# Kernel optimization log

Hardware: AMD Instinct MI355X
Metric: run time of the kernel (lower is better)

The kernel has to match this reference:

```python
import jax, jax.numpy as jnp
import numpy as np

# Module constants (from init_kwargs)
X_RANGE = (-10.0, 10.0)
Y_RANGE = (-10.0, 10.0)
N_X = 64
N_Y = 64
B = 16
N_CTX = 1024


def make_grid():
    # x counted forward, y counted backwards (image-row convention):
    # grid[k*N_X + j] = (xs[j], ys[k]) with ys from max to min.
    xs = jnp.linspace(X_RANGE[0], X_RANGE[1], N_X, dtype=jnp.float32)
    ys = jnp.linspace(Y_RANGE[1], Y_RANGE[0], N_Y, dtype=jnp.float32)
    gx, gy = jnp.meshgrid(xs, ys)          # each (N_Y, N_X)
    return jnp.stack([gx, gy], axis=-1).reshape(-1, 2)  # (G, 2)


def setup_inputs() -> dict:
    key = jax.random.key(0)
    k1, k2 = jax.random.split(key)
    X = jax.random.uniform(k1, (B, N_CTX, 2), dtype=jnp.float32,
                           minval=X_RANGE[0], maxval=X_RANGE[1])
    Y = jax.random.normal(k2, (B, N_CTX, 2), dtype=jnp.float32)
    log_l_scale = jnp.zeros((), dtype=jnp.float32)  # log(1.0)
    return {"X": X, "Y": Y, "log_l_scale": log_l_scale}


def reference(X, Y, log_l_scale):
    grid = make_grid()                                  # (G, 2)
    l = jnp.exp(log_l_scale)
    # squared distances via expansion to avoid a (B,G,n,2) intermediate
    g2 = jnp.sum(grid * grid, axis=-1)                  # (G,)
    x2 = jnp.sum(X * X, axis=-1)                        # (B, n)
    gx = jnp.einsum('gd,bnd->bgn', grid, X)             # (B, G, n)
    d2 = g2[None, :, None] + x2[:, None, :] - 2.0 * gx  # (B, G, n)
    Gram = jnp.exp(-0.5 * d2 / (l * l))                 # RBF kernel, B=1
    # expand Y with a leading ones (density) channel
    ones = jnp.ones(Y.shape[:2] + (1,), dtype=Y.dtype)
    EY = jnp.concatenate([ones, Y], axis=-1)            # (B, n, 3)
    FM = jnp.einsum('bgn,bnc->bgc', Gram, EY)           # (B, G, 3)
    dens = FM[..., 0:1]
    FM = jnp.concatenate([dens, FM[..., 1:] / dens], axis=-1)
    # (B, G, 3) -> (B, 3, N_Y, N_X)
    return FM.reshape(X.shape[0], N_Y, N_X, 3).transpose(0, 3, 1, 2)
```

## Files before the change

### kernel.cpp

```cpp
#include <hip/hip_runtime.h>
#include <hip/hip_bf16.h>
#include <math.h>

#define NB    16
#define NCTX  1024
#define NXG   64
#define NG    4096
#define GT_PER_B 16

__global__ __launch_bounds__(256)
void equiv_encoder_kernel(const float* __restrict__ X,
                          const float* __restrict__ Y,
                          const float* __restrict__ log_l_scale,
                          float* __restrict__ out) {
    const int b  = blockIdx.x >> 4;
    const int gt = blockIdx.x & 15;
    const int g  = gt * 256 + threadIdx.x;
    const int ix = g & 63;
    const int iy = g >> 6;

    const float step = 20.0f / 63.0f;
    const float gx = -10.0f + step * (float)ix;
    const float gy =  10.0f - step * (float)iy;

    const float logl  = log_l_scale[0];
    const float scale = -0.72134752044448170f * expf(-2.0f * logl);

    __shared__ float4 s[NCTX];
    const float2* Xb = (const float2*)(X + (size_t)b * NCTX * 2);
    const float2* Yb = (const float2*)(Y + (size_t)b * NCTX * 2);
    for (int i = threadIdx.x; i < NCTX; i += 256) {
        float2 xv = Xb[i];
        float2 yv = Yb[i];
        s[i] = make_float4(xv.x, xv.y, yv.x, yv.y);
    }
    __syncthreads();

    float a0 = 0.0f, a1 = 0.0f, a2 = 0.0f;
#pragma unroll 8
    for (int n = 0; n < NCTX; ++n) {
        float4 v = s[n];
        float dx = gx - v.x;
        float dy = gy - v.y;
        float d2 = fmaf(dx, dx, dy * dy);
        float w  = exp2f(d2 * scale);
        a0 += w;
        a1 = fmaf(w, v.z, a1);
        a2 = fmaf(w, v.w, a2);
    }

    const float inv = 1.0f / a0;
    float* ob = out + (size_t)b * 3 * NG;
    ob[g]            = a0;
    ob[NG + g]       = a1 * inv;
    ob[2 * NG + g]   = a2 * inv;
}

extern "C" void kernel_launch(void* const* d_in, const int* in_sizes, int n_in,
                              void* d_out, int out_size, void* d_ws, size_t ws_size,
                              hipStream_t stream) {
    const float* X    = (const float*)d_in[0];
    const float* Y    = (const float*)d_in[1];
    const float* logl = (const float*)d_in[2];
    float* out = (float*)d_out;

    dim3 grid(NB * GT_PER_B);
    dim3 block(256);
    equiv_encoder_kernel<<<grid, block, 0, stream>>>(X, Y, logl, out);
}
```

Measured before the change: 89.95 us.

## Factor RBF into separable x/y exponentials and split context across blocks

Uses the separability of the Gaussian on a regular grid, exp(-(dx²+dy²)) = exp(-dx²)·exp(-dy²), so per-axis weights are precomputed into shared memory and the inner loop becomes pure FMAs with no per-pair exp. Each thread now computes a 2x2 grid patch. The context dimension is split into 16 chunks across 1024 blocks, and a second kernel reduces the partials from workspace and normalizes. This removes the exp-bound inner loop and raises parallelism, in exchange for a second launch and workspace traffic.

```diff
diff --git a/kernel.cpp b/kernel.cpp
--- a/kernel.cpp
+++ b/kernel.cpp
@@ -2,58 +2,98 @@
 #include <hip/hip_bf16.h>
 #include <math.h>
 
-#define NB    16
-#define NCTX  1024
-#define NXG   64
-#define NG    4096
-#define GT_PER_B 16
+
+#define NB     16
+#define NCTX   1024
+#define NG     4096
+#define NC     64
+#define NSPLIT 16
+#define GQ     4
 
 __global__ __launch_bounds__(256)
-void equiv_encoder_kernel(const float* __restrict__ X,
-                          const float* __restrict__ Y,
-                          const float* __restrict__ log_l_scale,
-                          float* __restrict__ out) {
-    const int b  = blockIdx.x >> 4;
-    const int gt = blockIdx.x & 15;
-    const int g  = gt * 256 + threadIdx.x;
-    const int ix = g & 63;
-    const int iy = g >> 6;
+void ee_partial(const float* __restrict__ X,
+                const float* __restrict__ Y,
+                const float* __restrict__ log_l_scale,
+                float* __restrict__ ws) {
+    const int blk = blockIdx.x;
+    const int b   = blk >> 6;
+    const int r   = blk & 63;
+    const int gq  = r >> 4;
+    const int nc  = r & 15;
+    const int n0  = nc * NC;
+    const int iy0 = gq * 16;
 
-    const float step = 20.0f / 63.0f;
-    const float gx = -10.0f + step * (float)ix;
-    const float gy =  10.0f - step * (float)iy;
+    const float step  = 20.0f / 63.0f;
+    const float scale = -0.72134752044448170f * expf(-2.0f * log_l_scale[0]);
 
-    const float logl  = log_l_scale[0];
-    const float scale = -0.72134752044448170f * expf(-2.0f * logl);
+    __shared__ float  wx[NC][64];
+    __shared__ float  wy[NC][16];
+    __shared__ float2 sy[NC];
 
-    __shared__ float4 s[NCTX];
     const float2* Xb = (const float2*)(X + (size_t)b * NCTX * 2);
     const float2* Yb = (const float2*)(Y + (size_t)b * NCTX * 2);
-    for (int i = threadIdx.x; i < NCTX; i += 256) {
-        float2 xv = Xb[i];
-        float2 yv = Yb[i];
-        s[i] = make_float4(xv.x, xv.y, yv.x, yv.y);
+
+    for (int idx = threadIdx.x; idx < NC * 64; idx += 256) {
+        const int j = idx >> 6, i = idx & 63;
+        const float dx = (-10.0f + step * (float)i) - Xb[n0 + j].x;
+        wx[j][i] = exp2f(dx * dx * scale);
     }
+    for (int idx = threadIdx.x; idx < NC * 16; idx += 256) {
+        const int j = idx >> 4, q = idx & 15;
+        const float dy = (10.0f - step * (float)(iy0 + q)) - Xb[n0 + j].y;
+        wy[j][q] = exp2f(dy * dy * scale);
+    }
+    if (threadIdx.x < NC) sy[threadIdx.x] = Yb[n0 + threadIdx.x];
     __syncthreads();
 
-    float a0 = 0.0f, a1 = 0.0f, a2 = 0.0f;
-#pragma unroll 8
-    for (int n = 0; n < NCTX; ++n) {
-        float4 v = s[n];
-        float dx = gx - v.x;
-        float dy = gy - v.y;
-        float d2 = fmaf(dx, dx, dy * dy);
-        float w  = exp2f(d2 * scale);
-        a0 += w;
-        a1 = fmaf(w, v.z, a1);
-        a2 = fmaf(w, v.w, a2);
+    const int ixp = threadIdx.x & 31;
+    const int iyp = threadIdx.x >> 5;
+    float c00 = 0, c01 = 0, c02 = 0;
+    float c10 = 0, c11 = 0, c12 = 0;
+    float c20 = 0, c21 = 0, c22 = 0;
+    float c30 = 0, c31 = 0, c32 = 0;
+
+#pragma unroll 4
+    for (int n = 0; n < NC; ++n) {
+        const float2 wxv = *(const float2*)&wx[n][ixp * 2];
+        const float2 wyv = *(const float2*)&wy[n][iyp * 2];
+        const float2 yv  = sy[n];
+        const float pA0 = wyv.x * yv.x, pA1 = wyv.x * yv.y;
+        const float pB0 = wyv.y * yv.x, pB1 = wyv.y * yv.y;
+        c00 = fmaf(wxv.x, wyv.x, c00); c01 = fmaf(wxv.x, pA0, c01); c02 = fmaf(wxv.x, pA1, c02);
+        c10 = fmaf(wxv.y, wyv.x, c10); c11 = fmaf(wxv.y, pA0, c11); c12 = fmaf(wxv.y, pA1, c12);
+        c20 = fmaf(wxv.x, wyv.y, c20); c21 = fmaf(wxv.x, pB0, c21); c22 = fmaf(wxv.x, pB1, c22);
+        c30 = fmaf(wxv.y, wyv.y, c30); c31 = fmaf(wxv.y, pB0, c31); c32 = fmaf(wxv.y, pB1, c32);
     }
 
+    float* base = ws + (((size_t)(b * NSPLIT + nc)) * 3) * NG;
+    const int g0 = (iy0 + 2 * iyp) * 64 + 2 * ixp;
+    *(float2*)&base[g0]           = make_float2(c00, c10);
+    *(float2*)&base[g0 + 64]      = make_float2(c20, c30);
+    *(float2*)&base[NG + g0]      = make_float2(c01, c11);
+    *(float2*)&base[NG + g0 + 64] = make_float2(c21, c31);
+    *(float2*)&base[2*NG + g0]      = make_float2(c02, c12);
+    *(float2*)&base[2*NG + g0 + 64] = make_float2(c22, c32);
+}
+
+__global__ __launch_bounds__(256)
+void ee_reduce(const float* __restrict__ ws, float* __restrict__ out) {
+    const int t = blockIdx.x * 256 + threadIdx.x;
+    const int b = t >> 12, g = t & 4095;
+    const float* base = ws + (size_t)b * NSPLIT * 3 * NG;
+    float a0 = 0, a1 = 0, a2 = 0;
+#pragma unroll
+    for (int nc = 0; nc < NSPLIT; ++nc) {
+        const float* p = base + nc * 3 * NG;
+        a0 += p[g];
+        a1 += p[NG + g];
+        a2 += p[2 * NG + g];
+    }
     const float inv = 1.0f / a0;
     float* ob = out + (size_t)b * 3 * NG;
-    ob[g]            = a0;
-    ob[NG + g]       = a1 * inv;
-    ob[2 * NG + g]   = a2 * inv;
+    ob[g]          = a0;
+    ob[NG + g]     = a1 * inv;
+    ob[2 * NG + g] = a2 * inv;
 }
 
 extern "C" void kernel_launch(void* const* d_in, const int* in_sizes, int n_in,
@@ -63,8 +103,8 @@
     const float* Y    = (const float*)d_in[1];
     const float* logl = (const float*)d_in[2];
     float* out = (float*)d_out;
+    float* ws  = (float*)d_ws;
 
-    dim3 grid(NB * GT_PER_B);
-    dim3 block(256);
-    equiv_encoder_kernel<<<grid, block, 0, stream>>>(X, Y, logl, out);
+    ee_partial<<<dim3(NB * GQ * NSPLIT), dim3(256), 0, stream>>>(X, Y, logl, ws);
+    ee_reduce <<<dim3(NB * NG / 256),    dim3(256), 0, stream>>>(ws, out);
 }
```

Measured after the change: 72.90 us. 19.0% less time.

## Factor RBF kernel into separable x/y exponentials with double-buffered shared tables

Applied to the files above, without the earlier changes.

Uses exp(-(dx²+dy²)) = exp(-dx²)·exp(-dy²) so each block precomputes per-context x-weights for its 64 grid columns and y-weights (premultiplied by Y) for its 4 grid rows. These go into double-buffered shared-memory chunks of 64 context points. The inner loop becomes three FMAs per point with no exp, which removes the transcendental bottleneck. In exchange it adds chunked loads, table builds and a barrier per chunk, and the product of two separately rounded exponentials may differ slightly in numerics.

```diff
diff --git a/kernel.cpp b/kernel.cpp
--- a/kernel.cpp
+++ b/kernel.cpp
@@ -2,58 +2,85 @@
 #include <hip/hip_bf16.h>
 #include <math.h>
 
-#define NB    16
+
 #define NCTX  1024
-#define NXG   64
 #define NG    4096
-#define GT_PER_B 16
+#define NCH   64
+#define NCHUNK 16
 
 __global__ __launch_bounds__(256)
-void equiv_encoder_kernel(const float* __restrict__ X,
-                          const float* __restrict__ Y,
-                          const float* __restrict__ log_l_scale,
-                          float* __restrict__ out) {
-    const int b  = blockIdx.x >> 4;
-    const int gt = blockIdx.x & 15;
-    const int g  = gt * 256 + threadIdx.x;
-    const int ix = g & 63;
-    const int iy = g >> 6;
+void ee_fused(const float* __restrict__ X,
+              const float* __restrict__ Y,
+              const float* __restrict__ log_l_scale,
+              float* __restrict__ out) {
+    const int b   = blockIdx.x >> 4;
+    const int t   = blockIdx.x & 15;
+    const int iy0 = t * 4;
+    const int tid = threadIdx.x;
+    const int ix  = tid & 63;
+    const int iyl = tid >> 6;
 
-    const float step = 20.0f / 63.0f;
-    const float gx = -10.0f + step * (float)ix;
-    const float gy =  10.0f - step * (float)iy;
+    const float step  = 20.0f / 63.0f;
+    const float scale = -0.72134752044448170f * expf(-2.0f * log_l_scale[0]);
+    const float gx    = -10.0f + step * (float)ix;
 
-    const float logl  = log_l_scale[0];
-    const float scale = -0.72134752044448170f * expf(-2.0f * logl);
+    __shared__ float  wx [2][NCH][64];
+    __shared__ float4 wyt[2][NCH][4];
 
-    __shared__ float4 s[NCTX];
     const float2* Xb = (const float2*)(X + (size_t)b * NCTX * 2);
     const float2* Yb = (const float2*)(Y + (size_t)b * NCTX * 2);
-    for (int i = threadIdx.x; i < NCTX; i += 256) {
-        float2 xv = Xb[i];
-        float2 yv = Yb[i];
-        s[i] = make_float4(xv.x, xv.y, yv.x, yv.y);
-    }
+
+    float  xr[16];
+    float2 xw, yw;
+    const int jw = tid >> 2;
+    const int qw = tid & 3;
+    const float gyq = 10.0f - step * (float)(iy0 + qw);
+
+    auto load_chunk = [&](int c) {
+        const int n0 = c * NCH;
+#pragma unroll
+        for (int k = 0; k < 16; ++k)
+            xr[k] = Xb[n0 + (tid >> 6) + k * 4].x;
+        xw = Xb[n0 + jw];
+        yw = Yb[n0 + jw];
+    };
+    auto store_tables = [&](int p) {
+        const float dy = gyq - xw.y;
+        const float wy = exp2f(dy * dy * scale);
+        wyt[p][jw][qw] = make_float4(wy, wy * yw.x, wy * yw.y, 0.0f);
+#pragma unroll
+        for (int k = 0; k < 16; ++k) {
+            const float dx = gx - xr[k];
+            wx[p][(tid >> 6) + k * 4][ix] = exp2f(dx * dx * scale);
+        }
+    };
+
+    load_chunk(0);
+    store_tables(0);
     __syncthreads();
 
-    float a0 = 0.0f, a1 = 0.0f, a2 = 0.0f;
+    float d = 0.0f, a1 = 0.0f, a2 = 0.0f;
+    for (int c = 0; c < NCHUNK; ++c) {
+        const int p = c & 1;
+        if (c + 1 < NCHUNK) load_chunk(c + 1);
 #pragma unroll 8
-    for (int n = 0; n < NCTX; ++n) {
-        float4 v = s[n];
-        float dx = gx - v.x;
-        float dy = gy - v.y;
-        float d2 = fmaf(dx, dx, dy * dy);
-        float w  = exp2f(d2 * scale);
-        a0 += w;
-        a1 = fmaf(w, v.z, a1);
-        a2 = fmaf(w, v.w, a2);
+        for (int n = 0; n < NCH; ++n) {
+            const float  wxv = wx[p][n][ix];
+            const float4 wv  = wyt[p][n][iyl];
+            d  = fmaf(wxv, wv.x, d);
+            a1 = fmaf(wxv, wv.y, a1);
+            a2 = fmaf(wxv, wv.z, a2);
+        }
+        if (c + 1 < NCHUNK) store_tables(p ^ 1);
+        __syncthreads();
     }
 
-    const float inv = 1.0f / a0;
+    const int g = (iy0 + iyl) * 64 + ix;
+    const float inv = 1.0f / d;
     float* ob = out + (size_t)b * 3 * NG;
-    ob[g]            = a0;
-    ob[NG + g]       = a1 * inv;
-    ob[2 * NG + g]   = a2 * inv;
+    ob[g]          = d;
+    ob[NG + g]     = a1 * inv;
+    ob[2 * NG + g] = a2 * inv;
 }
 
 extern "C" void kernel_launch(void* const* d_in, const int* in_sizes, int n_in,
@@ -64,7 +91,5 @@
     const float* logl = (const float*)d_in[2];
     float* out = (float*)d_out;
 
-    dim3 grid(NB * GT_PER_B);
-    dim3 block(256);
-    equiv_encoder_kernel<<<grid, block, 0, stream>>>(X, Y, logl, out);
+    ee_fused<<<dim3(256), dim3(256), 0, stream>>>(X, Y, logl, out);
 }
```

Result: faster. 85.14 us (-5.3%).

## Split context points across four thread groups with shared-memory reduction

Applied to the files above, without the earlier changes.

Each block now uses 1024 threads. Four groups of 256 threads each handle a quarter of the context points for the same 256 grid cells, and their partial sums are combined through shared memory. The context values are read directly from global memory at wave-uniform addresses (readfirstlane), so they become scalar loads and the LDS staging pass goes away. This gives four times as many waves with a quarter of the serial loop each, at the cost of a reduction step and a single block per CU.

```diff
diff --git a/kernel.cpp b/kernel.cpp
--- a/kernel.cpp
+++ b/kernel.cpp
@@ -2,58 +2,73 @@
 #include <hip/hip_bf16.h>
 #include <math.h>
 
+
 #define NB    16
 #define NCTX  1024
-#define NXG   64
 #define NG    4096
-#define GT_PER_B 16
+#define NQ    4
+#define NPQ   (NCTX / NQ)
+#define CELLS 256
 
-__global__ __launch_bounds__(256)
-void equiv_encoder_kernel(const float* __restrict__ X,
-                          const float* __restrict__ Y,
-                          const float* __restrict__ log_l_scale,
-                          float* __restrict__ out) {
-    const int b  = blockIdx.x >> 4;
-    const int gt = blockIdx.x & 15;
-    const int g  = gt * 256 + threadIdx.x;
-    const int ix = g & 63;
-    const int iy = g >> 6;
+__global__ __launch_bounds__(1024, 1)
+void ee_single(const float* __restrict__ X,
+               const float* __restrict__ Y,
+               const float* __restrict__ log_l_scale,
+               float* __restrict__ out) {
+    const int b    = blockIdx.x >> 4;
+    const int tile = blockIdx.x & 15;
+    const int tid  = threadIdx.x;
+    const int c    = tid & 255;
+    const int q    = tid >> 8;
+    const int ix   = c & 63;
+    const int iy   = tile * 4 + (c >> 6);
 
-    const float step = 20.0f / 63.0f;
+    const float step  = 20.0f / 63.0f;
+    const float scale = -0.72134752044448170f * expf(-2.0f * log_l_scale[0]);
     const float gx = -10.0f + step * (float)ix;
     const float gy =  10.0f - step * (float)iy;
 
-    const float logl  = log_l_scale[0];
-    const float scale = -0.72134752044448170f * expf(-2.0f * logl);
+    const int n0 = __builtin_amdgcn_readfirstlane(q * NPQ);
 
-    __shared__ float4 s[NCTX];
     const float2* Xb = (const float2*)(X + (size_t)b * NCTX * 2);
     const float2* Yb = (const float2*)(Y + (size_t)b * NCTX * 2);
-    for (int i = threadIdx.x; i < NCTX; i += 256) {
-        float2 xv = Xb[i];
-        float2 yv = Yb[i];
-        s[i] = make_float4(xv.x, xv.y, yv.x, yv.y);
+
+    float d = 0.0f, a1 = 0.0f, a2 = 0.0f;
+#pragma unroll 8
+    for (int i = 0; i < NPQ; ++i) {
+        const float2 xv = Xb[n0 + i];
+        const float2 yv = Yb[n0 + i];
+        const float dx = gx - xv.x;
+        const float dy = gy - xv.y;
+        float d2 = dx * dx;
+        d2 = fmaf(dy, dy, d2);
+        const float w = exp2f(d2 * scale);
+        d  += w;
+        a1 = fmaf(w, yv.x, a1);
+        a2 = fmaf(w, yv.y, a2);
+    }
+
+    __shared__ float red[(NQ - 1) * CELLS * 3];
+    if (q > 0) {
+        float* r = &red[((q - 1) * CELLS + c) * 3];
+        r[0] = d; r[1] = a1; r[2] = a2;
     }
     __syncthreads();
-
-    float a0 = 0.0f, a1 = 0.0f, a2 = 0.0f;
-#pragma unroll 8
-    for (int n = 0; n < NCTX; ++n) {
-        float4 v = s[n];
-        float dx = gx - v.x;
-        float dy = gy - v.y;
-        float d2 = fmaf(dx, dx, dy * dy);
-        float w  = exp2f(d2 * scale);
-        a0 += w;
-        a1 = fmaf(w, v.z, a1);
-        a2 = fmaf(w, v.w, a2);
+    if (q == 0) {
+#pragma unroll
+        for (int k = 0; k < NQ - 1; ++k) {
+            const float* r = &red[(k * CELLS + c) * 3];
+            d  += r[0];
+            a1 += r[1];
+            a2 += r[2];
+        }
+        const int g = tile * 256 + c;
+        const float inv = 1.0f / d;
+        float* ob = out + (size_t)b * 3 * NG;
+        ob[g]          = d;
+        ob[NG + g]     = a1 * inv;
+        ob[2 * NG + g] = a2 * inv;
     }
-
-    const float inv = 1.0f / a0;
-    float* ob = out + (size_t)b * 3 * NG;
-    ob[g]            = a0;
-    ob[NG + g]       = a1 * inv;
-    ob[2 * NG + g]   = a2 * inv;
 }
 
 extern "C" void kernel_launch(void* const* d_in, const int* in_sizes, int n_in,
@@ -64,7 +79,5 @@
     const float* logl = (const float*)d_in[2];
     float* out = (float*)d_out;
 
-    dim3 grid(NB * GT_PER_B);
-    dim3 block(256);
-    equiv_encoder_kernel<<<grid, block, 0, stream>>>(X, Y, logl, out);
+    ee_single<<<dim3(NB * 16), dim3(1024), 0, stream>>>(X, Y, logl, out);
 }
```

New measurement: 85.33 us. 1.05x faster.
